# Kernel tuning notes

Hardware: AMD Instinct MI355X
Metric: run time of the kernel (lower is better)

## Reference

```python
import jax, jax.numpy as jnp
import numpy as np

B, N, N_FEAT = 16, 1024, 128
N_LAYER, AGG_HIDDEN, FC_HIDDEN, N_CLASS = 3, 64, 128, 10
NEG_INF = -9e15
LEAKY_SLOPE = 0.2


def setup_inputs() -> dict:
    key = jax.random.key(0)
    ks = jax.random.split(key, 8)
    x = jax.random.normal(ks[0], (B, N, N_FEAT), dtype=jnp.float32)
    adj = jax.random.randint(ks[1], (B, N, N), 0, 2).astype(jnp.float32)
    # per-layer GAT params, stacked over layers
    Ws = jax.random.normal(ks[2], (N_LAYER, N_FEAT, AGG_HIDDEN), dtype=jnp.float32) * 0.1
    a1 = jax.random.normal(ks[3], (N_LAYER, AGG_HIDDEN), dtype=jnp.float32) * 0.1
    a2 = jax.random.normal(ks[4], (N_LAYER, AGG_HIDDEN), dtype=jnp.float32) * 0.1
    W1 = jax.random.normal(ks[5], (AGG_HIDDEN * N_LAYER, FC_HIDDEN), dtype=jnp.float32) * 0.05
    b1 = jnp.zeros((FC_HIDDEN,), dtype=jnp.float32)
    W2 = jax.random.normal(ks[6], (FC_HIDDEN, N_CLASS), dtype=jnp.float32) * 0.05
    b2 = jnp.zeros((N_CLASS,), dtype=jnp.float32)
    return {"x": x, "adj": adj, "Ws": Ws, "a1": a1, "a2": a2,
            "W1": W1, "b1": b1, "W2": W2, "b2": b2}


def _gat_layer(x, adj, W, a1, a2):
    # h: [B, N, H]
    h = jnp.einsum('bnf,fh->bnh', x, W)
    # e_ij = LeakyReLU(a1.h_i + a2.h_j)  -- split-a trick, avoids [B,N,N,2H]
    f1 = jnp.einsum('bnh,h->bn', h, a1)
    f2 = jnp.einsum('bnh,h->bn', h, a2)
    e = jax.nn.leaky_relu(f1[:, :, None] + f2[:, None, :], LEAKY_SLOPE)  # [B,N,N]
    att = jax.nn.softmax(jnp.where(adj > 0, e, NEG_INF), axis=-1)
    return jnp.einsum('bnm,bmh->bnh', att, h)


def reference(x, adj, Ws, a1, a2, W1, b1, W2, b2):
    # eval mode: dropout is identity
    outs = [jax.nn.relu(_gat_layer(x, adj, Ws[i], a1[i], a2[i]))
            for i in range(N_LAYER)]
    h = jnp.concatenate(outs, axis=2)          # [B, N, H*L]
    pooled = jnp.mean(h, axis=1)               # 'avg' pool over nodes -> [B, H*L]
    z = jax.nn.relu(pooled @ W1 + b1)
    return jax.nn.softmax(z @ W2 + b2, axis=-1)  # [B, n_class]
```

## Files before the change

### kernel.cpp

```cpp
#include <hip/hip_runtime.h>

#define B 16
#define N 1024
#define NF 128
#define NL 3
#define AH 64
#define HC 192
#define FCH 128
#define NC 10
#define L2E 1.44269504088896f

typedef __attribute__((ext_vector_type(8))) short bf16x8;
typedef __attribute__((ext_vector_type(4))) float f32x4;
typedef __attribute__((ext_vector_type(4))) unsigned int u32x4;

static __device__ __forceinline__ unsigned short f2bf(float f) {
  unsigned int x = __builtin_bit_cast(unsigned int, f);
  return (unsigned short)((x + 0x7fffu + ((x >> 16) & 1u)) >> 16);
}
static __device__ __forceinline__ float bf2f(unsigned short u) {
  unsigned int x = ((unsigned int)u) << 16;
  return __builtin_bit_cast(float, x);
}

__global__ __launch_bounds__(256, 2) void k_feat(
    const float* __restrict__ x, const float* __restrict__ Ws,
    const float* __restrict__ a1, const float* __restrict__ a2,
    unsigned short* __restrict__ h_f, float* __restrict__ f1g,
    float* __restrict__ f2g, float* __restrict__ pooled)
{
  __shared__ float xs[64][132];
  __shared__ unsigned short wl[2][64][136];
  unsigned short (*hlds)[72] = (unsigned short(*)[72])&xs[0][0];
  const int t = threadIdx.x;
  const int n0g = blockIdx.x * 64;
  const int gb = n0g >> 10, nl0 = n0g & 1023;
  const int wv = t >> 6, lane = t & 63;
  const int lr = lane & 15, lg = lane >> 4;
  const int lrow = wv * 16 + lr;
  const int wcol = t & 63, woct = t >> 6;

  if (blockIdx.x == 0) {
    #pragma unroll
    for (int i = 0; i < 12; ++i) pooled[i * 256 + t] = 0.f;
  }

#define LOADW(R, L) {                                                         \
    _Pragma("unroll")                                                         \
    for (int p = 0; p < 4; ++p) {                                             \
      const int oct = p * 4 + woct;                                           \
      _Pragma("unroll")                                                       \
      for (int i = 0; i < 8; ++i)                                             \
        R[p][i] = Ws[((size_t)(L) * NF + oct * 8 + i) * AH + wcol];           \
    } }
#define WRITEW(R) {                                                           \
    _Pragma("unroll")                                                         \
    for (int p = 0; p < 4; ++p) {                                             \
      const int oct = p * 4 + woct;                                           \
      bf16x8 hv, lv;                                                          \
      _Pragma("unroll")                                                       \
      for (int i = 0; i < 8; ++i) {                                           \
        const unsigned short hi = f2bf(R[p][i]);                              \
        hv[i] = (short)hi;                                                    \
        lv[i] = (short)f2bf(R[p][i] - bf2f(hi));                              \
      }                                                                       \
      *(bf16x8*)&wl[0][wcol][oct * 8] = hv;                                   \
      *(bf16x8*)&wl[1][wcol][oct * 8] = lv;                                   \
    } }
#define MFMAL(L) {                                                            \
    _Pragma("unroll")                                                         \
    for (int n2 = 0; n2 < 4; ++n2) {                                          \
      const int n = (L) * 4 + n2;                                             \
      _Pragma("unroll")                                                       \
      for (int kf = 0; kf < 4; ++kf) {                                        \
        const bf16x8 whi = *(const bf16x8*)&wl[0][n2 * 16 + lr][kf * 32 + lg * 8]; \
        const bf16x8 wlo = *(const bf16x8*)&wl[1][n2 * 16 + lr][kf * 32 + lg * 8]; \
        acc[n] = __builtin_amdgcn_mfma_f32_16x16x32_bf16(xhi[kf], whi, acc[n], 0, 0, 0); \
        acc[n] = __builtin_amdgcn_mfma_f32_16x16x32_bf16(xhi[kf], wlo, acc[n], 0, 0, 0); \
        acc[n] = __builtin_amdgcn_mfma_f32_16x16x32_bf16(xlo[kf], whi, acc[n], 0, 0, 0); \
      }                                                                       \
    } }

  float wrA[4][8], wrB[4][8];
  LOADW(wrA, 0);

  #pragma unroll
  for (int p = 0; p < 8; ++p) {
    const int q = p * 256 + t;
    const int row = q >> 5, c4 = (q & 31) * 4;
    *(float4*)&xs[row][c4] = *(const float4*)&x[(size_t)(n0g + row) * NF + c4];
  }
  __syncthreads();

  bf16x8 xhi[4], xlo[4];
  #pragma unroll
  for (int kf = 0; kf < 4; ++kf) {
    const float4 q0 = *(const float4*)&xs[lrow][kf * 32 + lg * 8];
    const float4 q1 = *(const float4*)&xs[lrow][kf * 32 + lg * 8 + 4];
    const float xv[8] = {q0.x, q0.y, q0.z, q0.w, q1.x, q1.y, q1.z, q1.w};
    #pragma unroll
    for (int e = 0; e < 8; ++e) {
      const unsigned short hi = f2bf(xv[e]);
      xhi[kf][e] = (short)hi;
      xlo[kf][e] = (short)f2bf(xv[e] - bf2f(hi));
    }
  }

  f32x4 acc[12];
  #pragma unroll
  for (int n = 0; n < 12; ++n) acc[n] = (f32x4){0.f, 0.f, 0.f, 0.f};

  WRITEW(wrA);
  LOADW(wrB, 1);
  __syncthreads();
  MFMAL(0);
  __syncthreads();
  WRITEW(wrB);
  LOADW(wrA, 2);
  __syncthreads();
  MFMAL(1);
  __syncthreads();
  WRITEW(wrA);
  __syncthreads();
  MFMAL(2);

#undef LOADW
#undef WRITEW
#undef MFMAL

  float s1[3][4], s2[3][4];
  #pragma unroll
  for (int l = 0; l < 3; ++l)
    #pragma unroll
    for (int r = 0; r < 4; ++r) { s1[l][r] = 0.f; s2[l][r] = 0.f; }
  #pragma unroll
  for (int n = 0; n < 12; ++n) {
    const int col = n * 16 + lr;
    const float a1v = a1[col] * L2E, a2v = a2[col] * L2E;
    const int l = n >> 2;
    #pragma unroll
    for (int r = 0; r < 4; ++r) {
      s1[l][r] += acc[n][r] * a1v;
      s2[l][r] += acc[n][r] * a2v;
    }
  }
  #pragma unroll
  for (int off = 1; off < 16; off <<= 1)
    #pragma unroll
    for (int l = 0; l < 3; ++l)
      #pragma unroll
      for (int r = 0; r < 4; ++r) {
        s1[l][r] += __shfl_xor(s1[l][r], off);
        s2[l][r] += __shfl_xor(s2[l][r], off);
      }
  if (lr == 0) {
    #pragma unroll
    for (int l = 0; l < 3; ++l)
      #pragma unroll
      for (int r = 0; r < 4; ++r) {
        const int rw = n0g + wv * 16 + lg * 4 + r;
        f1g[(size_t)l * (B * N) + rw] = s1[l][r];
        f2g[(size_t)l * (B * N) + rw] = s2[l][r];
      }
  }

  __syncthreads();
  #pragma unroll
  for (int n = 0; n < 12; ++n) {
    const int col = n * 16 + lr;
    #pragma unroll
    for (int rp = 0; rp < 2; ++rp) {
      const unsigned int pr = (unsigned int)f2bf(acc[n][rp * 2]) |
                              ((unsigned int)f2bf(acc[n][rp * 2 + 1]) << 16);
      *(unsigned int*)&hlds[col][wv * 16 + lg * 4 + rp * 2] = pr;
    }
  }
  __syncthreads();
  #pragma unroll
  for (int p = 0; p < 6; ++p) {
    const int widx = p * 256 + t;
    const int lane_w = widx & 63;
    const int jb2 = (widx >> 6) & 1;
    const int n_w = (widx >> 7) & 3;
    const int l_w = widx >> 9;
    const int col = l_w * 64 + n_w * 16 + (lane_w & 15);
    const int jloc = jb2 * 32 + (lane_w >> 4) * 8;
    const size_t off =
        ((((size_t)(gb * 3 + l_w) * 4 + n_w) * 32 + (nl0 >> 5) + jb2) * 64 + lane_w) * 8;
    *(uint4*)&h_f[off] = *(const uint4*)&hlds[col][jloc];
  }
}

__global__ __launch_bounds__(192, 3) void k_att(
    const float* __restrict__ adj, const unsigned short* __restrict__ h_f,
    const float* __restrict__ f1, const float* __restrict__ f2,
    float* __restrict__ pooled)
{
  const int bid = blockIdx.x;
  const int blk = (bid & 7) * 128 + (bid >> 3);
  const int b = blk >> 6;
  const int i0 = (blk & 63) * 16;
  const int ph = ((bid * 5) & 7) * 128;
  const int t = threadIdx.x;
  const int l = t >> 6, lane = t & 63;
  const int lr = lane & 15, lg = lane >> 4;
  const int msh = (lg & 1) * 8;

  __shared__ float uvt[NL][2][N];
  __shared__ unsigned short sm[16][66];

  const float* ap = adj + ((size_t)(b * N + i0)) * N;
  for (int q = t; q < 1024; q += 192) {
    const int row = q >> 6, ch = q & 63;
    const float* p = ap + (size_t)row * N + ch * 16;
    unsigned int bits = 0;
    #pragma unroll
    for (int qq = 0; qq < 4; ++qq) {
      const uint4 u = *(const uint4*)(p + qq * 4);
      bits |= (u.x ? 1u : 0u) << (qq * 4 + 0);
      bits |= (u.y ? 1u : 0u) << (qq * 4 + 1);
      bits |= (u.z ? 1u : 0u) << (qq * 4 + 2);
      bits |= (u.w ? 1u : 0u) << (qq * 4 + 3);
    }
    sm[row][ch] = (unsigned short)bits;
  }

  const float* f2p = f2 + (size_t)l * (B * N) + b * N;
  float mx = -1e30f;
  #pragma unroll
  for (int ch = 0; ch < 4; ++ch) {
    const int jb = ch * 256 + lane * 4;
    const float4 q = *(const float4*)&f2p[jb];
    mx = fmaxf(mx, fmaxf(fmaxf(q.x, q.y), fmaxf(q.z, q.w)));
    *(float4*)&uvt[l][0][jb] =
        (float4){exp2f(q.x), exp2f(q.y), exp2f(q.z), exp2f(q.w)};
    *(float4*)&uvt[l][1][jb] =
        (float4){exp2f(0.2f * q.x), exp2f(0.2f * q.y), exp2f(0.2f * q.z), exp2f(0.2f * q.w)};
  }
  #pragma unroll
  for (int off = 1; off < 64; off <<= 1) mx = fmaxf(mx, __shfl_xor(mx, off));

  const float f1r = f1[(size_t)l * (B * N) + b * N + i0 + lr];
  const float tts = f1r + mx;
  const float sr = fmaxf(tts, 0.f) + 0.2f * fminf(tts, 0.f);
  const float A = exp2f(f1r - sr);
  const float C = exp2f(0.2f * f1r - sr);

  const unsigned short* hfb = h_f + ((size_t)(b * 3 + l)) * 65536;
  const float* ut = &uvt[l][0][0];
  const float* vt = &uvt[l][1][0];
  const bf16x8 ones = {(short)0x3F80, (short)0x3F80, (short)0x3F80, (short)0x3F80,
                       (short)0x3F80, (short)0x3F80, (short)0x3F80, (short)0x3F80};

  f32x4 acc[4];
  #pragma unroll
  for (int n = 0; n < 4; ++n) acc[n] = (f32x4){0.f, 0.f, 0.f, 0.f};
  f32x4 accd = (f32x4){0.f, 0.f, 0.f, 0.f};

  __syncthreads();

#define LOADJ(BUF, MW, J) {                                                   \
    const int jj = (J) & (N - 1);                                             \
    const int jt = jj >> 6;                                                   \
    const unsigned int s0 = sm[lr][jt * 4 + (lg >> 1)];                       \
    const unsigned int s1 = sm[lr][jt * 4 + 2 + (lg >> 1)];                   \
    MW = ((s0 >> msh) & 0xffu) | (((s1 >> msh) & 0xffu) << 8);                \
    _Pragma("unroll")                                                         \
    for (int q = 0; q < 8; ++q) {                                             \
      const int ks = q >> 2, n = q & 3;                                       \
      BUF[q] = *(const bf16x8*)&hfb[(((size_t)n * 32 + (jj >> 5) + ks) * 64 + \
                                     lane) * 8];                              \
    } }

#define COMPJ(BUF, MW, J) {                                                   \
    _Pragma("unroll")                                                         \
    for (int ks = 0; ks < 2; ++ks) {                                          \
      const int kb = ((J) & (N - 1)) + ks * 32 + lg * 8;                      \
      const float4 u0 = *(const float4*)&ut[kb];                              \
      const float4 u1 = *(const float4*)&ut[kb + 4];                          \
      const float4 v0 = *(const float4*)&vt[kb];                              \
      const float4 v1 = *(const float4*)&vt[kb + 4];                          \
      const unsigned int mby = ((MW) >> (ks * 8)) & 0xffu;                    \
      const float uu[8] = {u0.x, u0.y, u0.z, u0.w, u1.x, u1.y, u1.z, u1.w};   \
      const float vv[8] = {v0.x, v0.y, v0.z, v0.w, v1.x, v1.y, v1.z, v1.w};   \
      unsigned int pk[4];                                                     \
      _Pragma("unroll")                                                       \
      for (int ep = 0; ep < 4; ++ep) {                                        \
        unsigned int pr[2];                                                   \
        _Pragma("unroll")                                                     \
        for (int h = 0; h < 2; ++h) {                                         \
          const int e = ep * 2 + h;                                           \
                  \
          const float p = fmaxf(A * uu[e], C * vv[e]);                        \
          const unsigned int sel =                                            \
              (unsigned int)(((int)(mby << (31 - e))) >> 31);                 \
          pr[h] = (__builtin_bit_cast(unsigned int, p) + 0x8000u) & sel;      \
        }                                                                     \
        pk[ep] = __builtin_amdgcn_perm(pr[1], pr[0], 0x07060302u);            \
      }                                                                       \
      const u32x4 pkv = {pk[0], pk[1], pk[2], pk[3]};                         \
      const bf16x8 av = __builtin_bit_cast(bf16x8, pkv);                      \
      _Pragma("unroll")                                                       \
      for (int n = 0; n < 4; ++n)                                             \
        acc[n] = __builtin_amdgcn_mfma_f32_16x16x32_bf16(av, BUF[ks * 4 + n], \
                                                         acc[n], 0, 0, 0);    \
      accd = __builtin_amdgcn_mfma_f32_16x16x32_bf16(av, ones, accd, 0, 0, 0);\
    } }

#define SBAR __builtin_amdgcn_sched_barrier(0)

  bf16x8 bA[8], bB[8];
  unsigned int mwA, mwB;
  LOADJ(bA, mwA, ph);
  SBAR;
  for (int j0 = 0; j0 < N; j0 += 128) {
    LOADJ(bB, mwB, ph + j0 + 64);
    SBAR;
    COMPJ(bA, mwA, ph + j0);
    SBAR;
    LOADJ(bA, mwA, ph + j0 + 128);
    SBAR;
    COMPJ(bB, mwB, ph + j0 + 64);
    SBAR;
  }
#undef LOADJ
#undef COMPJ
#undef SBAR

  float dn[4];
  #pragma unroll
  for (int r = 0; r < 4; ++r) dn[r] = 1.f / fmaxf(accd[r], 1e-37f);

  #pragma unroll
  for (int n = 0; n < 4; ++n) {
    float csum = 0.f;
    #pragma unroll
    for (int r = 0; r < 4; ++r) csum += fmaxf(acc[n][r] * dn[r], 0.f);
    csum += __shfl_xor(csum, 16);
    csum += __shfl_xor(csum, 32);
    if (lg == 0) atomicAdd(&pooled[b * HC + l * 64 + n * 16 + lr], csum);
  }
}

__global__ __launch_bounds__(192) void k_head(
    const float* __restrict__ pooled_sums, const float* __restrict__ W1,
    const float* __restrict__ b1, const float* __restrict__ W2,
    const float* __restrict__ b2, float* __restrict__ out)
{
  const int b = blockIdx.x, t = threadIdx.x;
  __shared__ float pooled[HC];
  __shared__ float z[FCH];
  __shared__ float logits[NC];

  if (t < HC) pooled[t] = pooled_sums[b * HC + t] * (1.f / (float)N);
  __syncthreads();

  if (t < FCH) {
    float a = b1[t];
    #pragma unroll 4
    for (int f = 0; f < HC; ++f) a += pooled[f] * W1[(size_t)f * FCH + t];
    z[t] = a > 0.f ? a : 0.f;
  }
  __syncthreads();

  if (t < NC) {
    float a = b2[t];
    #pragma unroll 4
    for (int f = 0; f < FCH; ++f) a += z[f] * W2[(size_t)f * NC + t];
    logits[t] = a;
  }
  __syncthreads();

  if (t == 0) {
    float mxl = logits[0];
    for (int c = 1; c < NC; ++c) mxl = fmaxf(mxl, logits[c]);
    float e[NC], sum = 0.f;
    for (int c = 0; c < NC; ++c) { e[c] = __expf(logits[c] - mxl); sum += e[c]; }
    const float inv = 1.f / sum;
    for (int c = 0; c < NC; ++c) out[b * NC + c] = e[c] * inv;
  }
}

extern "C" void kernel_launch(void* const* d_in, const int* in_sizes, int n_in,
                              void* d_out, int out_size, void* d_ws, size_t ws_size,
                              hipStream_t stream)
{
  const float* x   = (const float*)d_in[0];
  const float* adj = (const float*)d_in[1];
  const float* Ws  = (const float*)d_in[2];
  const float* a1  = (const float*)d_in[3];
  const float* a2  = (const float*)d_in[4];
  const float* W1  = (const float*)d_in[5];
  const float* b1  = (const float*)d_in[6];
  const float* W2  = (const float*)d_in[7];
  const float* b2  = (const float*)d_in[8];
  float* out = (float*)d_out;

  unsigned short* h_f   = (unsigned short*)d_ws;
  float*          f1    = (float*)(h_f + (size_t)B * HC * N);
  float*          f2    = f1 + (size_t)NL * B * N;
  float*          pooled= f2 + (size_t)NL * B * N;

  k_feat<<<256, 256, 0, stream>>>(x, Ws, a1, a2, h_f, f1, f2, pooled);
  k_att <<<1024, 192, 0, stream>>>(adj, h_f, f1, f2, pooled);
  k_head<<<B, 192, 0, stream>>>(pooled, W1, b1, W2, b2, out);
}
```

Baseline: 69.97 us.

## Split attention key range across two waves per layer with LDS reduction

```diff
diff --git a/kernel.cpp b/kernel.cpp
--- a/kernel.cpp
+++ b/kernel.cpp
@@ -191,7 +191,7 @@
   }
 }
 
-__global__ __launch_bounds__(192, 3) void k_att(
+__global__ __launch_bounds__(384, 6) void k_att(
     const float* __restrict__ adj, const unsigned short* __restrict__ h_f,
     const float* __restrict__ f1, const float* __restrict__ f2,
     float* __restrict__ pooled)
@@ -200,17 +200,19 @@
   const int blk = (bid & 7) * 128 + (bid >> 3);
   const int b = blk >> 6;
   const int i0 = (blk & 63) * 16;
-  const int ph = ((bid * 5) & 7) * 128;
   const int t = threadIdx.x;
-  const int l = t >> 6, lane = t & 63;
+  const int w = t >> 6, lane = t & 63;
+  const int l = w >> 1, h = w & 1;
   const int lr = lane & 15, lg = lane >> 4;
   const int msh = (lg & 1) * 8;
-
-  __shared__ float uvt[NL][2][N];
+  const int base = h * 512;
+  const int ph = base + ((bid * 5) & 3) * 128;
+
+  __shared__ float pool[NL * 2 * N];
   __shared__ unsigned short sm[16][66];
 
   const float* ap = adj + ((size_t)(b * N + i0)) * N;
-  for (int q = t; q < 1024; q += 192) {
+  for (int q = t; q < 1024; q += 384) {
     const int row = q >> 6, ch = q & 63;
     const float* p = ap + (size_t)row * N + ch * 16;
     unsigned int bits = 0;
@@ -226,16 +228,20 @@
   }
 
   const float* f2p = f2 + (size_t)l * (B * N) + b * N;
+  float* ut = &pool[(l * 2 + 0) * N];
+  float* vt = &pool[(l * 2 + 1) * N];
   float mx = -1e30f;
   #pragma unroll
   for (int ch = 0; ch < 4; ++ch) {
     const int jb = ch * 256 + lane * 4;
     const float4 q = *(const float4*)&f2p[jb];
     mx = fmaxf(mx, fmaxf(fmaxf(q.x, q.y), fmaxf(q.z, q.w)));
-    *(float4*)&uvt[l][0][jb] =
-        (float4){exp2f(q.x), exp2f(q.y), exp2f(q.z), exp2f(q.w)};
-    *(float4*)&uvt[l][1][jb] =
-        (float4){exp2f(0.2f * q.x), exp2f(0.2f * q.y), exp2f(0.2f * q.z), exp2f(0.2f * q.w)};
+    if ((ch >> 1) == h) {
+      *(float4*)&ut[jb] =
+          (float4){exp2f(q.x), exp2f(q.y), exp2f(q.z), exp2f(q.w)};
+      *(float4*)&vt[jb] =
+          (float4){exp2f(0.2f * q.x), exp2f(0.2f * q.y), exp2f(0.2f * q.z), exp2f(0.2f * q.w)};
+    }
   }
   #pragma unroll
   for (int off = 1; off < 64; off <<= 1) mx = fmaxf(mx, __shfl_xor(mx, off));
@@ -247,8 +253,6 @@
   const float C = exp2f(0.2f * f1r - sr);
 
   const unsigned short* hfb = h_f + ((size_t)(b * 3 + l)) * 65536;
-  const float* ut = &uvt[l][0][0];
-  const float* vt = &uvt[l][1][0];
   const bf16x8 ones = {(short)0x3F80, (short)0x3F80, (short)0x3F80, (short)0x3F80,
                        (short)0x3F80, (short)0x3F80, (short)0x3F80, (short)0x3F80};
 
@@ -260,7 +264,7 @@
   __syncthreads();
 
 #define LOADJ(BUF, MW, J) {                                                   \
-    const int jj = (J) & (N - 1);                                             \
+    const int jj = base | ((J) & 511);                                        \
     const int jt = jj >> 6;                                                   \
     const unsigned int s0 = sm[lr][jt * 4 + (lg >> 1)];                       \
     const unsigned int s1 = sm[lr][jt * 4 + 2 + (lg >> 1)];                   \
@@ -273,9 +277,10 @@
     } }
 
 #define COMPJ(BUF, MW, J) {                                                   \
+    const int jjc = base | ((J) & 511);                                       \
     _Pragma("unroll")                                                         \
     for (int ks = 0; ks < 2; ++ks) {                                          \
-      const int kb = ((J) & (N - 1)) + ks * 32 + lg * 8;                      \
+      const int kb = jjc + ks * 32 + lg * 8;                                  \
       const float4 u0 = *(const float4*)&ut[kb];                              \
       const float4 u1 = *(const float4*)&ut[kb + 4];                          \
       const float4 v0 = *(const float4*)&vt[kb];                              \
@@ -288,13 +293,13 @@
       for (int ep = 0; ep < 4; ++ep) {                                        \
         unsigned int pr[2];                                                   \
         _Pragma("unroll")                                                     \
-        for (int h = 0; h < 2; ++h) {                                         \
-          const int e = ep * 2 + h;                                           \
+        for (int hh = 0; hh < 2; ++hh) {                                      \
+          const int e = ep * 2 + hh;                                          \
                   \
           const float p = fmaxf(A * uu[e], C * vv[e]);                        \
           const unsigned int sel =                                            \
               (unsigned int)(((int)(mby << (31 - e))) >> 31);                 \
-          pr[h] = (__builtin_bit_cast(unsigned int, p) + 0x8000u) & sel;      \
+          pr[hh] = (__builtin_bit_cast(unsigned int, p) + 0x8000u) & sel;     \
         }                                                                     \
         pk[ep] = __builtin_amdgcn_perm(pr[1], pr[0], 0x07060302u);            \
       }                                                                       \
@@ -313,7 +318,7 @@
   unsigned int mwA, mwB;
   LOADJ(bA, mwA, ph);
   SBAR;
-  for (int j0 = 0; j0 < N; j0 += 128) {
+  for (int j0 = 0; j0 < 512; j0 += 128) {
     LOADJ(bB, mwB, ph + j0 + 64);
     SBAR;
     COMPJ(bA, mwA, ph + j0);
@@ -327,18 +332,39 @@
 #undef COMPJ
 #undef SBAR
 
-  float dn[4];
-  #pragma unroll
-  for (int r = 0; r < 4; ++r) dn[r] = 1.f / fmaxf(accd[r], 1e-37f);
-
-  #pragma unroll
-  for (int n = 0; n < 4; ++n) {
-    float csum = 0.f;
-    #pragma unroll
-    for (int r = 0; r < 4; ++r) csum += fmaxf(acc[n][r] * dn[r], 0.f);
-    csum += __shfl_xor(csum, 16);
-    csum += __shfl_xor(csum, 32);
-    if (lg == 0) atomicAdd(&pooled[b * HC + l * 64 + n * 16 + lr], csum);
+  __syncthreads();
+  if (h == 1) {
+    float* dst = &pool[(l * 64 + lane) * 20];
+    #pragma unroll
+    for (int n = 0; n < 4; ++n)
+      #pragma unroll
+      for (int r = 0; r < 4; ++r) dst[n * 4 + r] = acc[n][r];
+    #pragma unroll
+    for (int r = 0; r < 4; ++r) dst[16 + r] = accd[r];
+  }
+  __syncthreads();
+  if (h == 0) {
+    const float* src = &pool[(l * 64 + lane) * 20];
+    #pragma unroll
+    for (int n = 0; n < 4; ++n)
+      #pragma unroll
+      for (int r = 0; r < 4; ++r) acc[n][r] += src[n * 4 + r];
+    #pragma unroll
+    for (int r = 0; r < 4; ++r) accd[r] += src[16 + r];
+
+    float dn[4];
+    #pragma unroll
+    for (int r = 0; r < 4; ++r) dn[r] = 1.f / fmaxf(accd[r], 1e-37f);
+
+    #pragma unroll
+    for (int n = 0; n < 4; ++n) {
+      float csum = 0.f;
+      #pragma unroll
+      for (int r = 0; r < 4; ++r) csum += fmaxf(acc[n][r] * dn[r], 0.f);
+      csum += __shfl_xor(csum, 16);
+      csum += __shfl_xor(csum, 32);
+      if (lg == 0) atomicAdd(&pooled[b * HC + l * 64 + n * 16 + lr], csum);
+    }
   }
 }
 
@@ -402,6 +428,6 @@
   float*          pooled= f2 + (size_t)NL * B * N;
 
   k_feat<<<256, 256, 0, stream>>>(x, Ws, a1, a2, h_f, f1, f2, pooled);
-  k_att <<<1024, 192, 0, stream>>>(adj, h_f, f1, f2, pooled);
+  k_att <<<1024, 384, 0, stream>>>(adj, h_f, f1, f2, pooled);
   k_head<<<B, 192, 0, stream>>>(pooled, W1, b1, W2, b2, out);
 }
```

Result: slower. 154.6 us (+121.0%).

## Stage attention B-operand tiles through LDS with direct global-to-LDS loads

Applied to the files above, without the earlier changes.

```diff
diff --git a/kernel.cpp b/kernel.cpp
--- a/kernel.cpp
+++ b/kernel.cpp
@@ -21,6 +21,13 @@
 static __device__ __forceinline__ float bf2f(unsigned short u) {
   unsigned int x = ((unsigned int)u) << 16;
   return __builtin_bit_cast(float, x);
+}
+
+static __device__ __forceinline__ void gload_lds16(const unsigned short* g,
+                                                   unsigned short* s) {
+  __builtin_amdgcn_global_load_lds(
+      (const __attribute__((address_space(1))) void*)g,
+      (__attribute__((address_space(3))) void*)s, 16, 0, 0);
 }
 
 __global__ __launch_bounds__(256, 2) void k_feat(
@@ -191,7 +198,7 @@
   }
 }
 
-__global__ __launch_bounds__(192, 3) void k_att(
+__global__ __launch_bounds__(192) void k_att(
     const float* __restrict__ adj, const unsigned short* __restrict__ h_f,
     const float* __restrict__ f1, const float* __restrict__ f2,
     float* __restrict__ pooled)
@@ -200,7 +207,6 @@
   const int blk = (bid & 7) * 128 + (bid >> 3);
   const int b = blk >> 6;
   const int i0 = (blk & 63) * 16;
-  const int ph = ((bid * 5) & 7) * 128;
   const int t = threadIdx.x;
   const int l = t >> 6, lane = t & 63;
   const int lr = lane & 15, lg = lane >> 4;
@@ -208,6 +214,7 @@
 
   __shared__ float uvt[NL][2][N];
   __shared__ unsigned short sm[16][66];
+  __shared__ unsigned short stage[NL][2][4096];
 
   const float* ap = adj + ((size_t)(b * N + i0)) * N;
   for (int q = t; q < 1024; q += 192) {
@@ -257,30 +264,42 @@
   for (int n = 0; n < 4; ++n) acc[n] = (f32x4){0.f, 0.f, 0.f, 0.f};
   f32x4 accd = (f32x4){0.f, 0.f, 0.f, 0.f};
 
-  __syncthreads();
-
-#define LOADJ(BUF, MW, J) {                                                   \
-    const int jj = (J) & (N - 1);                                             \
-    const int jt = jj >> 6;                                                   \
-    const unsigned int s0 = sm[lr][jt * 4 + (lg >> 1)];                       \
-    const unsigned int s1 = sm[lr][jt * 4 + 2 + (lg >> 1)];                   \
-    MW = ((s0 >> msh) & 0xffu) | (((s1 >> msh) & 0xffu) << 8);                \
+  const unsigned short* fp[8];
+  #pragma unroll
+  for (int q = 0; q < 8; ++q) {
+    const int ks = q >> 2, n = q & 3;
+    fp[q] = hfb + (((size_t)n * 32 + ks) * 64 + lane) * 8;
+  }
+
+  __syncthreads();
+
+#define ISSUE(BUFI) {                                                         \
     _Pragma("unroll")                                                         \
     for (int q = 0; q < 8; ++q) {                                             \
-      const int ks = q >> 2, n = q & 3;                                       \
-      BUF[q] = *(const bf16x8*)&hfb[(((size_t)n * 32 + (jj >> 5) + ks) * 64 + \
-                                     lane) * 8];                              \
+      gload_lds16(fp[q], &stage[l][BUFI][q * 512]);                           \
+      fp[q] += 1024;                                                          \
     } }
-
-#define COMPJ(BUF, MW, J) {                                                   \
+#define WAITC { asm volatile("s_waitcnt vmcnt(8)" ::: "memory");              \
+                __builtin_amdgcn_sched_barrier(0); }
+
+#define COMPJ(BUFI, J) {                                                      \
+    const unsigned short* sb = &stage[l][BUFI][lane * 8];                     \
+    bf16x8 bfr[8];                                                            \
+    _Pragma("unroll")                                                         \
+    for (int q = 0; q < 8; ++q)                                               \
+      bfr[q] = *(const bf16x8*)&sb[q * 512];                                  \
+    const int jt_ = (J) >> 6;                                                 \
+    const unsigned int s0_ = sm[lr][jt_ * 4 + (lg >> 1)];                     \
+    const unsigned int s1_ = sm[lr][jt_ * 4 + 2 + (lg >> 1)];                 \
+    const unsigned int MW = ((s0_ >> msh) & 0xffu) | (((s1_ >> msh) & 0xffu) << 8); \
     _Pragma("unroll")                                                         \
     for (int ks = 0; ks < 2; ++ks) {                                          \
-      const int kb = ((J) & (N - 1)) + ks * 32 + lg * 8;                      \
+      const int kb = (J) + ks * 32 + lg * 8;                                  \
       const float4 u0 = *(const float4*)&ut[kb];                              \
       const float4 u1 = *(const float4*)&ut[kb + 4];                          \
       const float4 v0 = *(const float4*)&vt[kb];                              \
       const float4 v1 = *(const float4*)&vt[kb + 4];                          \
-      const unsigned int mby = ((MW) >> (ks * 8)) & 0xffu;                    \
+      const unsigned int mby = (MW >> (ks * 8)) & 0xffu;                      \
       const float uu[8] = {u0.x, u0.y, u0.z, u0.w, u1.x, u1.y, u1.z, u1.w};   \
       const float vv[8] = {v0.x, v0.y, v0.z, v0.w, v1.x, v1.y, v1.z, v1.w};   \
       unsigned int pk[4];                                                     \
@@ -302,30 +321,23 @@
       const bf16x8 av = __builtin_bit_cast(bf16x8, pkv);                      \
       _Pragma("unroll")                                                       \
       for (int n = 0; n < 4; ++n)                                             \
-        acc[n] = __builtin_amdgcn_mfma_f32_16x16x32_bf16(av, BUF[ks * 4 + n], \
+        acc[n] = __builtin_amdgcn_mfma_f32_16x16x32_bf16(av, bfr[ks * 4 + n], \
                                                          acc[n], 0, 0, 0);    \
       accd = __builtin_amdgcn_mfma_f32_16x16x32_bf16(av, ones, accd, 0, 0, 0);\
     } }
 
-#define SBAR __builtin_amdgcn_sched_barrier(0)
-
-  bf16x8 bA[8], bB[8];
-  unsigned int mwA, mwB;
-  LOADJ(bA, mwA, ph);
-  SBAR;
-  for (int j0 = 0; j0 < N; j0 += 128) {
-    LOADJ(bB, mwB, ph + j0 + 64);
-    SBAR;
-    COMPJ(bA, mwA, ph + j0);
-    SBAR;
-    LOADJ(bA, mwA, ph + j0 + 128);
-    SBAR;
-    COMPJ(bB, mwB, ph + j0 + 64);
-    SBAR;
-  }
-#undef LOADJ
+  ISSUE(0);
+  for (int jt = 0; jt < 16; jt += 2) {
+    ISSUE(1);
+    WAITC;
+    COMPJ(0, jt * 64);
+    ISSUE(0);
+    WAITC;
+    COMPJ(1, jt * 64 + 64);
+  }
+#undef ISSUE
+#undef WAITC
 #undef COMPJ
-#undef SBAR
 
   float dn[4];
   #pragma unroll
```

After: 74.45 us. +6.4%, slower.

## Precompute exp tables in a separate kernel instead of per-block LDS setup

Applied to the files above, without the earlier changes.

```diff
diff --git a/kernel.cpp b/kernel.cpp
--- a/kernel.cpp
+++ b/kernel.cpp
@@ -191,22 +191,51 @@
   }
 }
 
-__global__ __launch_bounds__(192, 3) void k_att(
+__global__ __launch_bounds__(256) void k_tab(
+    const float* __restrict__ f1, const float* __restrict__ f2,
+    float* __restrict__ tab)
+{
+  __shared__ float red[4];
+  const int lb = blockIdx.x, t = threadIdx.x;
+  const float* f2p = f2 + (size_t)lb * N;
+  const float* f1p = f1 + (size_t)lb * N;
+
+  float v = -1e30f;
+  #pragma unroll
+  for (int i = 0; i < 4; ++i) v = fmaxf(v, f2p[i * 256 + t]);
+  #pragma unroll
+  for (int off = 32; off; off >>= 1) v = fmaxf(v, __shfl_down(v, off));
+  if ((t & 63) == 0) red[t >> 6] = v;
+  __syncthreads();
+  const float mx = fmaxf(fmaxf(red[0], red[1]), fmaxf(red[2], red[3]));
+
+  #pragma unroll
+  for (int i = 0; i < 4; ++i) {
+    const int j = i * 256 + t;
+    const float q2 = f2p[j];
+    const float q1 = f1p[j];
+    const float tt = q1 + mx;
+    const float sr = fmaxf(tt, 0.f) + 0.2f * fminf(tt, 0.f);
+    tab[(size_t)(0 * NL * B + lb) * N + j] = exp2f(q2);
+    tab[(size_t)(1 * NL * B + lb) * N + j] = exp2f(0.2f * q2);
+    tab[(size_t)(2 * NL * B + lb) * N + j] = exp2f(q1 - sr);
+    tab[(size_t)(3 * NL * B + lb) * N + j] = exp2f(0.2f * q1 - sr);
+  }
+}
+
+__global__ __launch_bounds__(192) void k_att(
     const float* __restrict__ adj, const unsigned short* __restrict__ h_f,
-    const float* __restrict__ f1, const float* __restrict__ f2,
-    float* __restrict__ pooled)
+    const float* __restrict__ tab, float* __restrict__ pooled)
 {
   const int bid = blockIdx.x;
   const int blk = (bid & 7) * 128 + (bid >> 3);
   const int b = blk >> 6;
   const int i0 = (blk & 63) * 16;
-  const int ph = ((bid * 5) & 7) * 128;
   const int t = threadIdx.x;
   const int l = t >> 6, lane = t & 63;
   const int lr = lane & 15, lg = lane >> 4;
   const int msh = (lg & 1) * 8;
 
-  __shared__ float uvt[NL][2][N];
   __shared__ unsigned short sm[16][66];
 
   const float* ap = adj + ((size_t)(b * N + i0)) * N;
@@ -225,30 +254,13 @@
     sm[row][ch] = (unsigned short)bits;
   }
 
-  const float* f2p = f2 + (size_t)l * (B * N) + b * N;
-  float mx = -1e30f;
-  #pragma unroll
-  for (int ch = 0; ch < 4; ++ch) {
-    const int jb = ch * 256 + lane * 4;
-    const float4 q = *(const float4*)&f2p[jb];
-    mx = fmaxf(mx, fmaxf(fmaxf(q.x, q.y), fmaxf(q.z, q.w)));
-    *(float4*)&uvt[l][0][jb] =
-        (float4){exp2f(q.x), exp2f(q.y), exp2f(q.z), exp2f(q.w)};
-    *(float4*)&uvt[l][1][jb] =
-        (float4){exp2f(0.2f * q.x), exp2f(0.2f * q.y), exp2f(0.2f * q.z), exp2f(0.2f * q.w)};
-  }
-  #pragma unroll
-  for (int off = 1; off < 64; off <<= 1) mx = fmaxf(mx, __shfl_xor(mx, off));
-
-  const float f1r = f1[(size_t)l * (B * N) + b * N + i0 + lr];
-  const float tts = f1r + mx;
-  const float sr = fmaxf(tts, 0.f) + 0.2f * fminf(tts, 0.f);
-  const float A = exp2f(f1r - sr);
-  const float C = exp2f(0.2f * f1r - sr);
+  const int lb = l * B + b;
+  const float* ut = tab + (size_t)(0 * NL * B + lb) * N;
+  const float* vt = tab + (size_t)(1 * NL * B + lb) * N;
+  const float A = tab[(size_t)(2 * NL * B + lb) * N + i0 + lr];
+  const float C = tab[(size_t)(3 * NL * B + lb) * N + i0 + lr];
 
   const unsigned short* hfb = h_f + ((size_t)(b * 3 + l)) * 65536;
-  const float* ut = &uvt[l][0][0];
-  const float* vt = &uvt[l][1][0];
   const bf16x8 ones = {(short)0x3F80, (short)0x3F80, (short)0x3F80, (short)0x3F80,
                        (short)0x3F80, (short)0x3F80, (short)0x3F80, (short)0x3F80};
 
@@ -311,16 +323,16 @@
 
   bf16x8 bA[8], bB[8];
   unsigned int mwA, mwB;
-  LOADJ(bA, mwA, ph);
+  LOADJ(bA, mwA, 0);
   SBAR;
   for (int j0 = 0; j0 < N; j0 += 128) {
-    LOADJ(bB, mwB, ph + j0 + 64);
+    LOADJ(bB, mwB, j0 + 64);
     SBAR;
-    COMPJ(bA, mwA, ph + j0);
+    COMPJ(bA, mwA, j0);
     SBAR;
-    LOADJ(bA, mwA, ph + j0 + 128);
+    LOADJ(bA, mwA, j0 + 128);
     SBAR;
-    COMPJ(bB, mwB, ph + j0 + 64);
+    COMPJ(bB, mwB, j0 + 64);
     SBAR;
   }
 #undef LOADJ
@@ -400,8 +412,10 @@
   float*          f1    = (float*)(h_f + (size_t)B * HC * N);
   float*          f2    = f1 + (size_t)NL * B * N;
   float*          pooled= f2 + (size_t)NL * B * N;
+  float*          tab   = pooled + B * HC + 16;
 
   k_feat<<<256, 256, 0, stream>>>(x, Ws, a1, a2, h_f, f1, f2, pooled);
-  k_att <<<1024, 192, 0, stream>>>(adj, h_f, f1, f2, pooled);
+  k_tab <<<NL * B, 256, 0, stream>>>(f1, f2, tab);
+  k_att <<<1024, 192, 0, stream>>>(adj, h_f, tab, pooled);
   k_head<<<B, 192, 0, stream>>>(pooled, W1, b1, W2, b2, out);
 }
```

Result: slower. 82.37 us (+17.7%).
